# Performance work log

Hardware: AMD Instinct MI355X
Metric: run time of the kernel (lower is better)

## Reference

```python
import jax, jax.numpy as jnp
import numpy as np

THRESHOLD = 0.2  # relation_threshold default
LN_EPS = 1e-5


def setup_inputs() -> dict:
    key = jax.random.key(0)
    ks = jax.random.split(key, 4)
    N1, N2, F, H, R = 256, 256, 512, 512, 4
    feats_img = jax.random.normal(ks[0], (N1, F), dtype=jnp.float32)
    feats_txt = jax.random.normal(ks[1], (N2, F), dtype=jnp.float32)
    # relation_projector params (R stacked copies of the 2-layer MLP)
    W1 = jax.random.normal(ks[2], (R, H, 2 * F), dtype=jnp.float32) / np.sqrt(2 * F)
    b1 = jnp.zeros((R, H), dtype=jnp.float32)
    gamma = jnp.ones((R, H), dtype=jnp.float32)
    beta = jnp.zeros((R, H), dtype=jnp.float32)
    w2 = jax.random.normal(ks[3], (R, H), dtype=jnp.float32) / np.sqrt(H)
    b2 = jnp.zeros((R,), dtype=jnp.float32)
    return {"feats_img": feats_img, "feats_txt": feats_txt, "W1": W1, "b1": b1,
            "gamma": gamma, "beta": beta, "w2": w2, "b2": b2}


def _relation_scores(x, W1, b1, gamma, beta, w2, b2):
    """Vectorized pairwise MLP: for each relation r, score[i,j] = MLP_r(cat(x_i, x_j)).
    Returns [N, N, R]."""
    N, F = x.shape
    R = W1.shape[0]
    Wl, Wr = W1[:, :, :F], W1[:, :, F:]  # Linear on concat = left half @ x_i + right half @ x_j
    scores = []
    for r in range(R):  # small fixed loop over relations keeps peak memory at one [N,N,H] block
        a = x @ Wl[r].T                                  # [N, H]
        b = x @ Wr[r].T                                  # [N, H]
        h = a[:, None, :] + b[None, :, :] + b1[r]        # [N, N, H]
        mu = h.mean(-1, keepdims=True)
        var = h.var(-1, keepdims=True)                   # biased var, matches torch LayerNorm
        hn = (h - mu) * jax.lax.rsqrt(var + LN_EPS) * gamma[r] + beta[r]
        s = jnp.maximum(hn, 0.0) @ w2[r] + b2[r]         # [N, N]
        scores.append(s)
    return jnp.stack(scores, axis=-1)                    # [N, N, R]


def reference(feats_img, feats_txt, W1, b1, gamma, beta, w2, b2):
    # node_features = cat over modalities (node_types is a static host-side list: omitted)
    x = jnp.concatenate([feats_img, feats_txt], axis=0)  # [N, F]
    S = _relation_scores(x, W1, b1, gamma, beta, w2, b2) # [N, N, R]
    best_rel = jnp.argmax(S, axis=-1).astype(jnp.int32)  # edge_types, dense form
    best_score = S.max(axis=-1)                          # edge_weights, dense form
    N = x.shape[0]
    diag = jnp.eye(N, dtype=bool)
    edge_mask = (~diag) & (best_score > THRESHOLD)       # dense encoding of edge_index
    return x, best_score, best_rel, edge_mask
```

## Files before the change

### kernel.cpp

```cpp
#include <hip/hip_runtime.h>
#include <math.h>


namespace {
constexpr size_t PLANE  = 512 * 512;
constexpr size_t OFF_A   = 0;
constexpr size_t OFF_B   = OFF_A + 4 * PLANE;
constexpr size_t OFF_DOT = OFF_B + 4 * PLANE;
constexpr size_t OFF_S   = OFF_DOT + 8 * PLANE;
constexpr size_t OFF_MA  = OFF_S + 8 * PLANE;
constexpr size_t OFF_QA  = OFF_MA + 2048;
constexpr size_t OFF_MB  = OFF_QA + 2048;
constexpr size_t OFF_QB  = OFF_MB + 2048;
constexpr size_t OFF_G   = OFF_QB + 2048;
constexpr size_t OFF_BW  = OFF_G + 2048;
constexpr size_t OFF_SA  = OFF_BW + 4096;
constexpr size_t OFF_SB  = OFF_SA + 2048;
constexpr size_t OFF_CB  = OFF_SB + 2048;
}

__global__ __launch_bounds__(256) void k0_gemm(const float* __restrict__ img,
                                               const float* __restrict__ txt,
                                               const float* __restrict__ W1,
                                               const float* __restrict__ b1,
                                               float* __restrict__ ws) {
  const int b = blockIdx.x;
  const int it = b >> 6;
  const int ct = b & 63;
  const int which = ct >> 5;
  const int r = (ct >> 3) & 3;
  const int ht = ct & 7;
  const int i0 = it << 6, h0 = ht << 6;
  const int t = threadIdx.x;
  const int tx = t & 15, ty = t >> 4;

  __shared__ float Xs[16 * 68];
  __shared__ float Wsm[16 * 68];

  float acc[16], pacc[16];
#pragma unroll
  for (int p = 0; p < 16; ++p) { acc[p] = 0.f; pacc[p] = 0.f; }

  const int srow = t >> 2;
  const int sf4 = (t & 3) << 2;
  const int xi = i0 + srow;
  const float* xrow = (xi < 256) ? (img + (size_t)xi * 512)
                                 : (txt + (size_t)(xi - 256) * 512);
  const float* wrow = W1 + (size_t)(r * 512 + h0 + srow) * 1024 + which * 512;

  for (int k0 = 0; k0 < 512; k0 += 16) {
    const float4 xv = *(const float4*)(xrow + k0 + sf4);
    const float4 wv = *(const float4*)(wrow + k0 + sf4);
    __syncthreads();
    Xs[(sf4 + 0) * 68 + srow] = xv.x;
    Xs[(sf4 + 1) * 68 + srow] = xv.y;
    Xs[(sf4 + 2) * 68 + srow] = xv.z;
    Xs[(sf4 + 3) * 68 + srow] = xv.w;
    Wsm[(sf4 + 0) * 68 + srow] = wv.x;
    Wsm[(sf4 + 1) * 68 + srow] = wv.y;
    Wsm[(sf4 + 2) * 68 + srow] = wv.z;
    Wsm[(sf4 + 3) * 68 + srow] = wv.w;
    __syncthreads();
#pragma unroll
    for (int k = 0; k < 16; ++k) {
      const float4 a4 = *(const float4*)&Xs[k * 68 + 4 * ty];
      const float4 b4 = *(const float4*)&Wsm[k * 68 + 4 * tx];
      const float av[4] = {a4.x, a4.y, a4.z, a4.w};
      const float bv[4] = {b4.x, b4.y, b4.z, b4.w};
#pragma unroll
      for (int c = 0; c < 4; ++c)
#pragma unroll
        for (int d = 0; d < 4; ++d)
          pacc[c * 4 + d] = fmaf(av[c], bv[d], pacc[c * 4 + d]);
    }
#pragma unroll
    for (int p = 0; p < 16; ++p) { acc[p] += pacc[p]; pacc[p] = 0.f; }
  }

  float4 bb = make_float4(0.f, 0.f, 0.f, 0.f);
  if (which) bb = *(const float4*)(b1 + r * 512 + h0 + 4 * tx);
  float* dst = ws + (which ? OFF_B : OFF_A) + (size_t)r * PLANE;
#pragma unroll
  for (int c = 0; c < 4; ++c) {
    float4 v;
    v.x = acc[c * 4 + 0] + bb.x;
    v.y = acc[c * 4 + 1] + bb.y;
    v.z = acc[c * 4 + 2] + bb.z;
    v.w = acc[c * 4 + 3] + bb.w;
    *(float4*)(dst + (size_t)(i0 + 4 * ty + c) * 512 + h0 + 4 * tx) = v;
  }
}

__global__ __launch_bounds__(256) void k1_stats(float* __restrict__ ws,
                                                const float* __restrict__ gamma,
                                                const float* __restrict__ beta,
                                                const float* __restrict__ w2) {
  const int t = threadIdx.x;
  const int gw = (blockIdx.x * 256 + t) >> 6;
  const int lane = t & 63;
  const int which = gw >> 11;
  const int rr = (gw >> 9) & 3;
  const int row = gw & 511;
  const float* src =
      ws + (which ? OFF_B : OFF_A) + (size_t)(rr * 512 + row) * 512 + lane * 8;
  const float* gsrc = gamma + rr * 512 + lane * 8;
  const float* wsrc = w2 + rr * 512 + lane * 8;
  float s = 0.f, q = 0.f, sa = 0.f, cgs = 0.f;
#pragma unroll
  for (int c = 0; c < 2; ++c) {
    const float4 v = *(const float4*)(src + c * 4);
    const float4 g = *(const float4*)(gsrc + c * 4);
    const float4 w = *(const float4*)(wsrc + c * 4);
    s += v.x + v.y + v.z + v.w;
    q += v.x * v.x + v.y * v.y + v.z * v.z + v.w * v.w;
    const float cgx = 0.5f * w.x * g.x;
    const float cgy = 0.5f * w.y * g.y;
    const float cgz = 0.5f * w.z * g.z;
    const float cgw = 0.5f * w.w * g.w;
    sa += cgx * v.x + cgy * v.y + cgz * v.z + cgw * v.w;
    cgs += cgx + cgy + cgz + cgw;
  }
#pragma unroll
  for (int off = 32; off >= 1; off >>= 1) {
    s += __shfl_down(s, off, 64);
    q += __shfl_down(q, off, 64);
    sa += __shfl_down(sa, off, 64);
    cgs += __shfl_down(cgs, off, 64);
  }
  if (lane == 0) {
    const float ma = s * (1.f / 512.f);
    ws[(which ? OFF_MB : OFF_MA) + rr * 512 + row] = ma;
    ws[(which ? OFF_QB : OFF_QA) + rr * 512 + row] = q;
    ws[(which ? OFF_SB : OFF_SA) + rr * 512 + row] = sa - ma * cgs;
  }
  if (blockIdx.x < 8) {
    const int idx = blockIdx.x * 256 + t;
    ws[OFF_G + idx] = gamma[idx];
    float2 bw;
    bw.x = beta[idx];
    bw.y = 0.5f * w2[idx];
    *(float2*)(ws + OFF_BW + (size_t)idx * 2) = bw;
  }
  if (blockIdx.x == 8) {
    const int rb = t >> 6;
    float cb = 0.f;
#pragma unroll
    for (int c = 0; c < 8; ++c)
      cb += 0.5f * w2[rb * 512 + lane * 8 + c] * beta[rb * 512 + lane * 8 + c];
#pragma unroll
    for (int off = 32; off >= 1; off >>= 1) cb += __shfl_down(cb, off, 64);
    if (lane == 0) ws[OFF_CB + rb] = cb;
  }
}

__global__ __launch_bounds__(256) void k2_dot(float* __restrict__ ws) {
  const int b = blockIdx.x;
  const int jt = b & 7, it = (b >> 3) & 7, r = (b >> 6) & 3, ks = b >> 8;
  const int i0 = it << 6, j0 = jt << 6;
  const int kb = ks << 8;
  const int t = threadIdx.x;
  const int tx = t & 15, ty = t >> 4;

  __shared__ float As[16 * 68];
  __shared__ float Bs[16 * 68];

  float acc[16];
#pragma unroll
  for (int p = 0; p < 16; ++p) acc[p] = 0.f;

  const int srow = t >> 2, sf4 = (t & 3) << 2;
  const float* arow = ws + OFF_A + (size_t)(r * 512 + i0 + srow) * 512 + kb;
  const float* brow = ws + OFF_B + (size_t)(r * 512 + j0 + srow) * 512 + kb;

  for (int k0 = 0; k0 < 256; k0 += 16) {
    const float4 av = *(const float4*)(arow + k0 + sf4);
    const float4 bv = *(const float4*)(brow + k0 + sf4);
    __syncthreads();
    As[(sf4 + 0) * 68 + srow] = av.x;
    As[(sf4 + 1) * 68 + srow] = av.y;
    As[(sf4 + 2) * 68 + srow] = av.z;
    As[(sf4 + 3) * 68 + srow] = av.w;
    Bs[(sf4 + 0) * 68 + srow] = bv.x;
    Bs[(sf4 + 1) * 68 + srow] = bv.y;
    Bs[(sf4 + 2) * 68 + srow] = bv.z;
    Bs[(sf4 + 3) * 68 + srow] = bv.w;
    __syncthreads();
#pragma unroll
    for (int k = 0; k < 16; ++k) {
      const float4 a4 = *(const float4*)&As[k * 68 + 4 * ty];
      const float4 b4 = *(const float4*)&Bs[k * 68 + 4 * tx];
      const float av2[4] = {a4.x, a4.y, a4.z, a4.w};
      const float bv2[4] = {b4.x, b4.y, b4.z, b4.w};
#pragma unroll
      for (int c = 0; c < 4; ++c)
#pragma unroll
        for (int d = 0; d < 4; ++d)
          acc[c * 4 + d] = fmaf(av2[c], bv2[d], acc[c * 4 + d]);
    }
  }
  float* dst = ws + OFF_DOT + (size_t)ks * (4 * PLANE) + (size_t)r * PLANE;
#pragma unroll
  for (int c = 0; c < 4; ++c) {
    float4 v;
    v.x = acc[c * 4 + 0]; v.y = acc[c * 4 + 1];
    v.z = acc[c * 4 + 2]; v.w = acc[c * 4 + 3];
    *(float4*)(dst + (size_t)(i0 + 4 * ty + c) * 512 + j0 + 4 * tx) = v;
  }
}

__global__ __launch_bounds__(256) void k3_score(float* __restrict__ ws) {
  const int b = blockIdx.x;
  const int jt = b & 15, it = (b >> 4) & 7, r = (b >> 7) & 3, ks = b >> 9;
  const int i0 = it << 6, j0 = jt << 5;
  const int t = threadIdx.x;
  const int tx = t & 15, ty = t >> 4;

  __shared__ float As2[64 * 68];
  __shared__ float Bs2[64 * 36];
  __shared__ float bwS[64 * 2];

  const float4 mav = *(const float4*)(ws + OFF_MA + r * 512 + i0 + 4 * ty);
  const float4 qav = *(const float4*)(ws + OFF_QA + r * 512 + i0 + 4 * ty);
  const float2 mbv = *(const float2*)(ws + OFF_MB + r * 512 + j0 + 2 * tx);
  const float2 qbv = *(const float2*)(ws + OFF_QB + r * 512 + j0 + 2 * tx);
  const float4 sav = *(const float4*)(ws + OFF_SA + r * 512 + i0 + 4 * ty);
  const float2 sbv = *(const float2*)(ws + OFF_SB + r * 512 + j0 + 2 * tx);
  const float cbr = ws[OFF_CB + r];
  const float mavA[4] = {mav.x, mav.y, mav.z, mav.w};
  const float qavA[4] = {qav.x, qav.y, qav.z, qav.w};
  const float savA[4] = {sav.x, sav.y, sav.z, sav.w};
  const float mbA[2] = {mbv.x, mbv.y};
  const float qbA[2] = {qbv.x, qbv.y};
  const float sbA[2] = {sbv.x, sbv.y};
  float Sv[8], acc[8];
#pragma unroll
  for (int c = 0; c < 4; ++c) {
    const size_t doff = (size_t)r * PLANE + (size_t)(i0 + 4 * ty + c) * 512 + j0 + 2 * tx;
    const float2 d0 = *(const float2*)(ws + OFF_DOT + doff);
    const float2 d1 = *(const float2*)(ws + OFF_DOT + 4 * PLANE + doff);
    const float dA[2] = {d0.x + d1.x, d0.y + d1.y};
#pragma unroll
    for (int d = 0; d < 2; ++d) {
      const int p = c * 2 + d;
      const float mu = mavA[c] + mbA[d];
      const float msq = (qavA[c] + qbA[d] + 2.f * dA[d]) * (1.f / 512.f);
      const float var = msq - mu * mu;
      Sv[p] = 1.0f / sqrtf(var + 1e-5f);
      acc[p] = (ks == 0) ? fmaf(Sv[p], savA[c] + sbA[d], cbr) : 0.f;
    }
  }

  const int kbase = ks << 8;
  const int srow = ty;
  const int sf4 = tx << 2;
  const int sblk = tx & 7;
  float maR[4], mbR[2];
#pragma unroll
  for (int c2 = 0; c2 < 4; ++c2)
    maR[c2] = ws[OFF_MA + r * 512 + i0 + srow + 16 * c2];
#pragma unroll
  for (int c2 = 0; c2 < 2; ++c2)
    mbR[c2] = ws[OFF_MB + r * 512 + j0 + srow + 16 * c2];

  float4 aC[4], bC[2], gC;
  float2 bwC = make_float2(0.f, 0.f);
  {
    const int kb = kbase;
    gC = *(const float4*)(ws + OFF_G + r * 512 + kb + sf4);
#pragma unroll
    for (int c2 = 0; c2 < 4; ++c2)
      aC[c2] = *(const float4*)(ws + OFF_A + (size_t)(r * 512 + i0 + srow + 16 * c2) * 512 + kb + sf4);
#pragma unroll
    for (int c2 = 0; c2 < 2; ++c2)
      bC[c2] = *(const float4*)(ws + OFF_B + (size_t)(r * 512 + j0 + srow + 16 * c2) * 512 + kb + sf4);
    if (t < 64) bwC = *(const float2*)(ws + OFF_BW + (size_t)(r * 512 + kb + t) * 2);
  }

#pragma unroll
  for (int kc = 0; kc < 4; ++kc) {
    __syncthreads();
    {
      const float ga[4] = {gC.x, gC.y, gC.z, gC.w};
#pragma unroll
      for (int c2 = 0; c2 < 4; ++c2) {
        const int row = srow + 16 * c2;
        const int off = (((row >> 2) ^ sblk) << 2) + (row & 3);
        const float aq[4] = {aC[c2].x, aC[c2].y, aC[c2].z, aC[c2].w};
#pragma unroll
        for (int q = 0; q < 4; ++q)
          As2[(sf4 + q) * 68 + off] = (aq[q] - maR[c2]) * ga[q];
      }
#pragma unroll
      for (int c2 = 0; c2 < 2; ++c2) {
        const int row = srow + 16 * c2;
        const int off = (((row >> 2) ^ sblk) << 2) + (row & 3);
        const float bq[4] = {bC[c2].x, bC[c2].y, bC[c2].z, bC[c2].w};
#pragma unroll
        for (int q = 0; q < 4; ++q)
          Bs2[(sf4 + q) * 36 + off] = (bq[q] - mbR[c2]) * ga[q];
      }
      if (t < 64) *(float2*)(bwS + 2 * t) = bwC;
    }
    if (kc < 3) {
      const int kb = kbase + ((kc + 1) << 6);
      gC = *(const float4*)(ws + OFF_G + r * 512 + kb + sf4);
#pragma unroll
      for (int c2 = 0; c2 < 4; ++c2)
        aC[c2] = *(const float4*)(ws + OFF_A + (size_t)(r * 512 + i0 + srow + 16 * c2) * 512 + kb + sf4);
#pragma unroll
      for (int c2 = 0; c2 < 2; ++c2)
        bC[c2] = *(const float4*)(ws + OFF_B + (size_t)(r * 512 + j0 + srow + 16 * c2) * 512 + kb + sf4);
      if (t < 64) bwC = *(const float2*)(ws + OFF_BW + (size_t)(r * 512 + kb + t) * 2);
    }
    __syncthreads();

    float cacc[8];
#pragma unroll
    for (int p = 0; p < 8; ++p) cacc[p] = 0.f;

#pragma unroll 4
    for (int k = 0; k < 64; ++k) {
      const int K = (k >> 2) & 7;
      const float4 aA = *(const float4*)&As2[k * 68 + ((ty ^ K) << 2)];
      const float2 bB = *(const float2*)&Bs2[k * 36 + (((tx >> 1) ^ K) << 2) + ((tx & 1) << 1)];
      const float2 bw = *(const float2*)&bwS[2 * k];
      const float aq[4] = {aA.x, aA.y, aA.z, aA.w};
      const float bq[2] = {bB.x, bB.y};
#pragma unroll
      for (int c = 0; c < 4; ++c)
#pragma unroll
        for (int d = 0; d < 2; ++d) {
          const int p = c * 2 + d;
          const float u = aq[c] + bq[d];
          const float hn = fmaf(u, Sv[p], bw.x);
          cacc[p] = fmaf(bw.y, fabsf(hn), cacc[p]);
        }
    }
#pragma unroll
    for (int p = 0; p < 8; ++p) acc[p] += cacc[p];
  }

  float* dst = ws + OFF_S + (size_t)ks * (4 * PLANE) + (size_t)r * PLANE;
#pragma unroll
  for (int c = 0; c < 4; ++c) {
    float2 v;
    v.x = acc[c * 2 + 0];
    v.y = acc[c * 2 + 1];
    *(float2*)(dst + (size_t)(i0 + 4 * ty + c) * 512 + j0 + 2 * tx) = v;
  }
}

__global__ __launch_bounds__(256) void k4_combine(const float* __restrict__ ws,
                                                  const float* __restrict__ img,
                                                  const float* __restrict__ txt,
                                                  const float* __restrict__ b2,
                                                  float* __restrict__ out) {
  const int idx = blockIdx.x * 256 + threadIdx.x;
  const int i = idx >> 9, j = idx & 511;
  const float* s0 = ws + OFF_S;
  const float* s1 = ws + OFF_S + 4 * PLANE;
  float best = -3.4e38f;
  int rel = 0;
#pragma unroll
  for (int r = 0; r < 4; ++r) {
    const float s = s0[r * PLANE + idx] + s1[r * PLANE + idx] + b2[r];
    if (s > best) { best = s; rel = r; }
  }
  out[idx] = (i < 256) ? img[idx] : txt[idx - 131072];
  out[PLANE + idx] = best;
  out[2 * PLANE + idx] = (float)rel;
  out[3 * PLANE + idx] = (i != j && (double)best > 0.2) ? 1.0f : 0.0f;
}

extern "C" void kernel_launch(void* const* d_in, const int* in_sizes, int n_in,
                              void* d_out, int out_size, void* d_ws, size_t ws_size,
                              hipStream_t stream) {
  const float* img   = (const float*)d_in[0];
  const float* txt   = (const float*)d_in[1];
  const float* W1    = (const float*)d_in[2];
  const float* b1    = (const float*)d_in[3];
  const float* gamma = (const float*)d_in[4];
  const float* beta  = (const float*)d_in[5];
  const float* w2    = (const float*)d_in[6];
  const float* b2    = (const float*)d_in[7];
  float* ws  = (float*)d_ws;
  float* out = (float*)d_out;
  (void)in_sizes; (void)n_in; (void)out_size; (void)ws_size;

  hipLaunchKernelGGL(k0_gemm,    dim3(512),  dim3(256), 0, stream, img, txt, W1, b1, ws);
  hipLaunchKernelGGL(k1_stats,   dim3(1024), dim3(256), 0, stream, ws, gamma, beta, w2);
  hipLaunchKernelGGL(k2_dot,     dim3(512),  dim3(256), 0, stream, ws);
  hipLaunchKernelGGL(k3_score,   dim3(1024), dim3(256), 0, stream, ws);
  hipLaunchKernelGGL(k4_combine, dim3(1024), dim3(256), 0, stream, ws, img, txt, b2, out);
}
```

Measured before the change: 191.9 us.

## Replace FP32 dot GEMM with split-bf16 MFMA using a conversion pass

Adds a conversion kernel that splits the A and B projections into high and low bf16 halves, stored in the OFF_S workspace region. The pairwise dot-product kernel now uses 16x16x32 bf16 MFMA with three products (hh, hl, lh) to approximate FP32 accuracy. This replaces the scalar FMA shared-memory GEMM with matrix-core instructions, at the cost of an extra launch and extra memory traffic for the converted copies. The MFMA kernel loads straight from global memory without LDS staging and writes scalar, column-strided outputs. It also relies on OFF_S being free at this point, before k3 uses it.

```diff
diff --git a/kernel.cpp b/kernel.cpp
--- a/kernel.cpp
+++ b/kernel.cpp
@@ -1,6 +1,10 @@
 #include <hip/hip_runtime.h>
 #include <math.h>
 
+
+typedef __attribute__((ext_vector_type(8))) short s8b;
+typedef __attribute__((ext_vector_type(4))) float f32x4;
+typedef __attribute__((ext_vector_type(4))) unsigned short us4;
 
 namespace {
 constexpr size_t PLANE  = 512 * 512;
@@ -19,6 +23,15 @@
 constexpr size_t OFF_CB  = OFF_SB + 2048;
 }
 
+__device__ __forceinline__ unsigned short bf16rne(float v) {
+  const unsigned u = __float_as_uint(v);
+  return (unsigned short)((u + 0x7fffu + ((u >> 16) & 1u)) >> 16);
+}
+
+__device__ __forceinline__ f32x4 mfma16(s8b a, s8b b, f32x4 c) {
+  return __builtin_amdgcn_mfma_f32_16x16x32_bf16(a, b, c, 0, 0, 0);
+}
+
 __global__ __launch_bounds__(256) void k0_gemm(const float* __restrict__ img,
                                                const float* __restrict__ txt,
                                                const float* __restrict__ W1,
@@ -89,6 +102,30 @@
     v.w = acc[c * 4 + 3] + bb.w;
     *(float4*)(dst + (size_t)(i0 + 4 * ty + c) * 512 + h0 + 4 * tx) = v;
   }
+}
+
+__global__ __launch_bounds__(256) void k_conv2(float* __restrict__ ws) {
+  const int idx = blockIdx.x * 256 + threadIdx.x;
+  const float4 v = *(const float4*)(ws + (size_t)idx * 4);
+  unsigned short* SH = (unsigned short*)(ws + OFF_S);
+  unsigned short *dh, *dl;
+  if (idx < 262144) {
+    const size_t e = (size_t)idx * 4;
+    dh = SH + e;                 dl = SH + 4 * PLANE + e;
+  } else {
+    const size_t e = (size_t)idx * 4 - 4 * PLANE;
+    dh = SH + 8 * PLANE + e;     dl = SH + 12 * PLANE + e;
+  }
+  const float vv[4] = {v.x, v.y, v.z, v.w};
+  us4 h4, l4;
+#pragma unroll
+  for (int c = 0; c < 4; ++c) {
+    const unsigned short hh = bf16rne(vv[c]);
+    h4[c] = hh;
+    l4[c] = bf16rne(vv[c] - __uint_as_float(((unsigned)hh) << 16));
+  }
+  *(us4*)dh = h4;
+  *(us4*)dl = l4;
 }
 
 __global__ __launch_bounds__(256) void k1_stats(float* __restrict__ ws,
@@ -153,58 +190,63 @@
   }
 }
 
-__global__ __launch_bounds__(256) void k2_dot(float* __restrict__ ws) {
+__global__ __launch_bounds__(256) void k2_mfma(float* __restrict__ ws) {
   const int b = blockIdx.x;
   const int jt = b & 7, it = (b >> 3) & 7, r = (b >> 6) & 3, ks = b >> 8;
   const int i0 = it << 6, j0 = jt << 6;
   const int kb = ks << 8;
-  const int t = threadIdx.x;
-  const int tx = t & 15, ty = t >> 4;
-
-  __shared__ float As[16 * 68];
-  __shared__ float Bs[16 * 68];
-
-  float acc[16];
-#pragma unroll
-  for (int p = 0; p < 16; ++p) acc[p] = 0.f;
-
-  const int srow = t >> 2, sf4 = (t & 3) << 2;
-  const float* arow = ws + OFF_A + (size_t)(r * 512 + i0 + srow) * 512 + kb;
-  const float* brow = ws + OFF_B + (size_t)(r * 512 + j0 + srow) * 512 + kb;
-
-  for (int k0 = 0; k0 < 256; k0 += 16) {
-    const float4 av = *(const float4*)(arow + k0 + sf4);
-    const float4 bv = *(const float4*)(brow + k0 + sf4);
-    __syncthreads();
-    As[(sf4 + 0) * 68 + srow] = av.x;
-    As[(sf4 + 1) * 68 + srow] = av.y;
-    As[(sf4 + 2) * 68 + srow] = av.z;
-    As[(sf4 + 3) * 68 + srow] = av.w;
-    Bs[(sf4 + 0) * 68 + srow] = bv.x;
-    Bs[(sf4 + 1) * 68 + srow] = bv.y;
-    Bs[(sf4 + 2) * 68 + srow] = bv.z;
-    Bs[(sf4 + 3) * 68 + srow] = bv.w;
-    __syncthreads();
-#pragma unroll
-    for (int k = 0; k < 16; ++k) {
-      const float4 a4 = *(const float4*)&As[k * 68 + 4 * ty];
-      const float4 b4 = *(const float4*)&Bs[k * 68 + 4 * tx];
-      const float av2[4] = {a4.x, a4.y, a4.z, a4.w};
-      const float bv2[4] = {b4.x, b4.y, b4.z, b4.w};
-#pragma unroll
-      for (int c = 0; c < 4; ++c)
-#pragma unroll
-        for (int d = 0; d < 4; ++d)
-          acc[c * 4 + d] = fmaf(av2[c], bv2[d], acc[c * 4 + d]);
-    }
-  }
+  const int t = threadIdx.x, w = t >> 6, l = t & 63;
+  const int wr = w >> 1, wc = w & 1;
+  const int lrow = l & 15, lk = (l >> 4) << 3;
+
+  const unsigned short* SH = (const unsigned short*)(ws + OFF_S);
+  const unsigned short* AH = SH;
+  const unsigned short* AL = SH + 4 * PLANE;
+  const unsigned short* BH = SH + 8 * PLANE;
+  const unsigned short* BL = SH + 12 * PLANE;
+
+  const int ia = i0 + wr * 32 + lrow;
+  const int jb = j0 + wc * 32 + lrow;
+  const size_t ar0 = (size_t)(r * 512 + ia) * 512 + kb + lk;
+  const size_t ar1 = ar0 + 16 * 512;
+  const size_t br0 = (size_t)(r * 512 + jb) * 512 + kb + lk;
+  const size_t br1 = br0 + 16 * 512;
+
+  f32x4 acc00 = {0.f, 0.f, 0.f, 0.f}, acc01 = acc00, acc10 = acc00, acc11 = acc00;
+
+#pragma unroll
+  for (int k0 = 0; k0 < 256; k0 += 32) {
+    const s8b ah0 = *(const s8b*)(AH + ar0 + k0);
+    const s8b ah1 = *(const s8b*)(AH + ar1 + k0);
+    const s8b al0 = *(const s8b*)(AL + ar0 + k0);
+    const s8b al1 = *(const s8b*)(AL + ar1 + k0);
+    const s8b bh0 = *(const s8b*)(BH + br0 + k0);
+    const s8b bh1 = *(const s8b*)(BH + br1 + k0);
+    const s8b bl0 = *(const s8b*)(BL + br0 + k0);
+    const s8b bl1 = *(const s8b*)(BL + br1 + k0);
+    acc00 = mfma16(ah0, bh0, acc00);
+    acc00 = mfma16(ah0, bl0, acc00);
+    acc00 = mfma16(al0, bh0, acc00);
+    acc01 = mfma16(ah0, bh1, acc01);
+    acc01 = mfma16(ah0, bl1, acc01);
+    acc01 = mfma16(al0, bh1, acc01);
+    acc10 = mfma16(ah1, bh0, acc10);
+    acc10 = mfma16(ah1, bl0, acc10);
+    acc10 = mfma16(al1, bh0, acc10);
+    acc11 = mfma16(ah1, bh1, acc11);
+    acc11 = mfma16(ah1, bl1, acc11);
+    acc11 = mfma16(al1, bh1, acc11);
+  }
+
   float* dst = ws + OFF_DOT + (size_t)ks * (4 * PLANE) + (size_t)r * PLANE;
-#pragma unroll
-  for (int c = 0; c < 4; ++c) {
-    float4 v;
-    v.x = acc[c * 4 + 0]; v.y = acc[c * 4 + 1];
-    v.z = acc[c * 4 + 2]; v.w = acc[c * 4 + 3];
-    *(float4*)(dst + (size_t)(i0 + 4 * ty + c) * 512 + j0 + 4 * tx) = v;
+  const int rb = i0 + wr * 32 + ((l >> 4) << 2);
+  const int cb = j0 + wc * 32 + lrow;
+#pragma unroll
+  for (int v = 0; v < 4; ++v) {
+    dst[(size_t)(rb + v) * 512 + cb]           = acc00[v];
+    dst[(size_t)(rb + v) * 512 + cb + 16]      = acc01[v];
+    dst[(size_t)(rb + 16 + v) * 512 + cb]      = acc10[v];
+    dst[(size_t)(rb + 16 + v) * 512 + cb + 16] = acc11[v];
   }
 }
 
@@ -388,8 +430,9 @@
   (void)in_sizes; (void)n_in; (void)out_size; (void)ws_size;
 
   hipLaunchKernelGGL(k0_gemm,    dim3(512),  dim3(256), 0, stream, img, txt, W1, b1, ws);
+  hipLaunchKernelGGL(k_conv2,    dim3(2048), dim3(256), 0, stream, ws);
   hipLaunchKernelGGL(k1_stats,   dim3(1024), dim3(256), 0, stream, ws, gamma, beta, w2);
-  hipLaunchKernelGGL(k2_dot,     dim3(512),  dim3(256), 0, stream, ws);
+  hipLaunchKernelGGL(k2_mfma,    dim3(512),  dim3(256), 0, stream, ws);
   hipLaunchKernelGGL(k3_score,   dim3(1024), dim3(256), 0, stream, ws);
   hipLaunchKernelGGL(k4_combine, dim3(1024), dim3(256), 0, stream, ws, img, txt, b2, out);
 }
```

After: 192.7 us. Within noise of the previous version (+0.4%).
